# Kernel tuning notes

Hardware: AMD Instinct MI355X
Metric: run time of the kernel (lower is better)

The kernel has to match this reference:

```python
import jax, jax.numpy as jnp
import numpy as np

N_NODES = 20000
N_GRAPH = 256
NODE_DIM = 128
MULS = (128, 64, 32)       # node irreps: 128x0e + 64x1o + 32x2e
HC = 32                    # hidden channels per irrep
HIDDEN_DIM = 64
N_PATH = 9                 # feasible uuw paths into 0e+1e+2e
W_NUMEL = N_PATH * HC * HC # 9216


def _tables():
    # real Clebsch-Gordan tensors built from cartesian tensor algebra,
    # normalized so that sum(C**2) = 2*l_out + 1 (component normalization)
    eps = np.zeros((3, 3, 3))
    eps[0, 1, 2] = eps[1, 2, 0] = eps[2, 0, 1] = 1.0
    eps[0, 2, 1] = eps[2, 1, 0] = eps[1, 0, 2] = -1.0
    s2, s6 = 1 / np.sqrt(2), 1 / np.sqrt(6)
    Q2 = np.zeros((5, 3, 3))  # orthonormal basis of traceless symmetric 3x3
    Q2[0, 0, 1] = Q2[0, 1, 0] = s2          # xy
    Q2[1, 1, 2] = Q2[1, 2, 1] = s2          # yz
    Q2[2, 0, 0] = Q2[2, 1, 1] = -s6; Q2[2, 2, 2] = 2 * s6  # z2
    Q2[3, 0, 2] = Q2[3, 2, 0] = s2          # xz
    Q2[4, 0, 0] = s2; Q2[4, 1, 1] = -s2     # x2-y2

    def nrm(C, l3):
        return C * np.sqrt((2 * l3 + 1) / (C ** 2).sum())

    C000 = np.ones((1, 1, 1))
    C022 = np.eye(5)[None, :, :]
    C110 = np.eye(3).reshape(3, 3, 1) / np.sqrt(3)
    C111 = eps / np.sqrt(2)
    C112 = np.transpose(Q2, (1, 2, 0))
    C202 = np.eye(5)[:, None, :]
    C220 = np.eye(5).reshape(5, 5, 1) / np.sqrt(5)
    M = np.einsum('iab,jdb->ijad', Q2, Q2)  # [5,5,3,3]
    C221 = nrm(np.einsum('cad,ijad->ijc', eps, M), 1)
    S = 0.5 * (M + np.transpose(M, (0, 1, 3, 2)))
    S = S - np.trace(S, axis1=2, axis2=3)[..., None, None] * np.eye(3) / 3.0
    C222 = nrm(np.einsum('kad,ijad->ijk', Q2, S), 2)
    # sph2cart change of basis: 9 spherical comps (0e+1e+2e) -> 3x3 cartesian
    Qc = np.zeros((3, 3, 9))
    Qc[:, :, 0] = np.eye(3) / np.sqrt(3)        # isotropic part
    Qc[:, :, 1:4] = eps / np.sqrt(2)            # antisymmetric part
    Qc[:, :, 4:9] = np.transpose(Q2, (1, 2, 0)) # symmetric traceless part
    return [C000, C022, C110, C111, C112, C202, C220, C221, C222], Qc

_CGS, _QC = _tables()


def setup_inputs() -> dict:
    key = jax.random.key(0)
    ks = jax.random.split(key, 12)
    f32 = jnp.float32
    d_sph = MULS[0] + 3 * MULS[1] + 5 * MULS[2]  # 480
    return {
        'x_scalar': jax.random.normal(ks[0], (N_NODES, NODE_DIM), f32),
        'x_spherical': jax.random.normal(ks[1], (N_NODES, d_sph), f32),
        'batch': jnp.sort(jax.random.randint(ks[2], (N_NODES,), 0, N_GRAPH)),
        'W0e': jax.random.normal(ks[3], (MULS[0], HC), f32),
        'W1o': jax.random.normal(ks[4], (MULS[1], HC), f32),
        'W2e': jax.random.normal(ks[5], (MULS[2], HC), f32),
        'Wm1': jax.random.normal(ks[6], (NODE_DIM, HIDDEN_DIM), f32) / np.sqrt(NODE_DIM),
        'bm1': jnp.zeros((HIDDEN_DIM,), f32),
        'Wm2': jax.random.normal(ks[7], (HIDDEN_DIM, W_NUMEL), f32) / np.sqrt(HIDDEN_DIM),
        'bm2': jnp.zeros((W_NUMEL,), f32),
        'P0': jax.random.normal(ks[8], (3 * HC,), f32),
        'P1': jax.random.normal(ks[9], (2 * HC,), f32),
        'P2': jax.random.normal(ks[10], (4 * HC,), f32),
    }


def reference(x_scalar, x_spherical, batch, W0e, W1o, W2e, Wm1, bm1, Wm2, bm2, P0, P1, P2):
    n = x_scalar.shape[0]
    m0, m1, m2 = MULS
    # split node features into irrep blocks
    x0 = x_spherical[:, :m0, None]                        # [N,128,1] 0e
    x1 = x_spherical[:, m0:m0 + 3 * m1].reshape(n, m1, 3) # [N,64,3]  1o
    x2 = x_spherical[:, m0 + 3 * m1:].reshape(n, m2, 5)   # [N,32,5]  2e
    # pre_lin: per-irrep channel mixing (e3nn-style 1/sqrt(fan_in))
    h = [jnp.einsum('num,uv->nvm', x, W) / np.sqrt(W.shape[0])
         for x, W in ((x0, W0e), (x1, W1o), (x2, W2e))]   # each [N,32,2l+1]
    # per-node tensor-product weights from scalar features
    w = (jax.nn.silu(x_scalar @ Wm1 + bm1) @ Wm2 + bm2).reshape(n, N_PATH, HC, HC)
    # uuw tensor product, path order matches _CGS
    paths = ((0, 0), (0, 2), (1, 1), (1, 1), (1, 1), (2, 0), (2, 2), (2, 2), (2, 2))
    inv_u = 1.0 / np.sqrt(HC)
    outs = []
    for k, (i, j) in enumerate(paths):
        C = jnp.asarray(_CGS[k], x_scalar.dtype)
        outs.append(jnp.einsum('pqr,nup,nuq,nuw->nwr', C, h[i], h[j], w[:, k]) * inv_u)
    # post_lin: combine paths of each output l into a single channel
    y0 = jnp.einsum('num,u->nm', jnp.concatenate([outs[0], outs[2], outs[6]], 1), P0) / np.sqrt(3 * HC)
    y1 = jnp.einsum('num,u->nm', jnp.concatenate([outs[3], outs[7]], 1), P1) / np.sqrt(2 * HC)
    y2 = jnp.einsum('num,u->nm', jnp.concatenate([outs[1], outs[4], outs[5], outs[8]], 1), P2) / np.sqrt(4 * HC)
    sph = jnp.concatenate([y0, y1, y2], axis=1)           # [N,9]
    cart = jnp.einsum('abi,ni->nab', jnp.asarray(_QC, sph.dtype), sph)  # [N,3,3]
    red = jax.ops.segment_sum(cart, batch, num_segments=N_GRAPH)        # [B,3,3]
    # if_trace is False (if_iso=False): roll every non-batch dim by 1
    return jnp.roll(jnp.roll(red, 1, axis=1), 1, axis=2)
```

## Files before the change

### kernel.cpp

```cpp
#include <hip/hip_runtime.h>
#include <math.h>

#define OFF_W2P 0
#define OFF_B2P 14336
#define WS_FLOATS 14592

#define SC_Y0 0.0180421959121758f
#define SC_Y2 0.015625f
#define S2f 0.70710678118654752f
#define S6f 0.40824829046386302f
#define TWOS2f 1.41421356237309505f
#define TWOS6f 0.81649658092772603f
#define ISQRT3 0.57735026918962576f
#define ISQRT5 0.44721359549995794f
#define H0SC 0.08838834764831845f
#define H1SC 0.125f
#define H2SC 0.17677669529663689f

__device__ __constant__ int KARR[7] = {0, 1, 2, 4, 5, 6, 8};

__global__ __launch_bounds__(256) void prep_kernel(
    const float* __restrict__ Wm2, const float* __restrict__ bm2,
    const float* __restrict__ P0, const float* __restrict__ P2,
    float* __restrict__ ws, float* __restrict__ out) {
  int j = blockIdx.x * 256 + threadIdx.x;
  if (j < 2304) out[j] = 0.f;

  if (j < 14336) {
    int s = j >> 11; int rem = j & 2047; int c = rem >> 5; int u = rem & 31;
    int k = KARR[s];
    const float* P;
    float sc;
    switch (s) {
      case 0: P = P0;      sc = SC_Y0; break;
      case 1: P = P2;      sc = SC_Y2; break;
      case 2: P = P0 + 32; sc = SC_Y0; break;
      case 3: P = P2 + 32; sc = SC_Y2; break;
      case 4: P = P2 + 64; sc = SC_Y2; break;
      case 5: P = P0 + 64; sc = SC_Y0; break;
      default: P = P2 + 96; sc = SC_Y2; break;
    }
    const float4* w4 = (const float4*)(Wm2 + c * 9216 + k * 1024 + u * 32);
    const float4* p4 = (const float4*)P;
    float acc = 0.f;
#pragma unroll
    for (int q = 0; q < 8; ++q) {
      float4 a = w4[q], b = p4[q];
      acc += a.x * b.x + a.y * b.y + a.z * b.z + a.w * b.w;
    }
    ws[OFF_W2P + c * 224 + s * 32 + u] = acc * sc;
  } else if (j < 14560) {
    int i = j - 14336; int s = i >> 5; int u = i & 31; int k = KARR[s];
    const float* P;
    float sc;
    switch (s) {
      case 0: P = P0;      sc = SC_Y0; break;
      case 1: P = P2;      sc = SC_Y2; break;
      case 2: P = P0 + 32; sc = SC_Y0; break;
      case 3: P = P2 + 32; sc = SC_Y2; break;
      case 4: P = P2 + 64; sc = SC_Y2; break;
      case 5: P = P0 + 64; sc = SC_Y0; break;
      default: P = P2 + 96; sc = SC_Y2; break;
    }
    const float* b = bm2 + k * 1024 + u * 32;
    float acc = 0.f;
#pragma unroll
    for (int w = 0; w < 32; ++w) acc += b[w] * P[w];
    ws[OFF_B2P + s * 32 + u] = acc * sc;
  }
}

__global__ __launch_bounds__(256, 3) void fused_kernel(
    const float* __restrict__ xs_g, const float* __restrict__ xsph,
    const float* __restrict__ W0e, const float* __restrict__ W1o,
    const float* __restrict__ W2e,
    const float* __restrict__ Wm1, const float* __restrict__ bm1,
    const float* __restrict__ ws, const int* __restrict__ batch,
    float* __restrict__ out, const float norm2) {
  __shared__ __align__(16) char smem[50560];
  float (*xs)[132] = (float (*)[132])smem;
  float (*Vt)[228] = (float (*)[228])smem;
  float (*xp)[484] = (float (*)[484])(smem + 14592);
  float (*hiT)[18] = (float (*)[18])(smem + 45568);
  float (*sphs)[6] = (float (*)[6])(smem + 50176);

  const int tid = threadIdx.x;
  const int n0 = blockIdx.x * 16;

  for (int idx = tid; idx < 512; idx += 256) {
    const int row = idx >> 5, c4 = idx & 31;
    *(float4*)&xs[row][c4 * 4] = *(const float4*)(xs_g + (size_t)(n0 + row) * 128 + c4 * 4);
  }
  for (int idx = tid; idx < 1920; idx += 256) {
    const int row = idx / 120, c4 = idx % 120;
    *(float4*)&xp[row][c4 * 4] = *(const float4*)(xsph + (size_t)(n0 + row) * 480 + c4 * 4);
  }
  __syncthreads();

  {
    const int n = tid >> 4, c0 = (tid & 15) * 4;
    float acc[4] = {0.f, 0.f, 0.f, 0.f};
#pragma unroll 4
    for (int mq = 0; mq < 32; ++mq) {
      const float4 xv = *(float4*)&xs[n][mq * 4];
      const float xa[4] = {xv.x, xv.y, xv.z, xv.w};
#pragma unroll
      for (int r = 0; r < 4; ++r) {
        const float4 w = *(const float4*)(Wm1 + (mq * 4 + r) * 64 + c0);
        const float xr = xa[r];
        acc[0] += xr * w.x; acc[1] += xr * w.y;
        acc[2] += xr * w.z; acc[3] += xr * w.w;
      }
    }
    const float4 bb = *(const float4*)(bm1 + c0);
    const float ba[4] = {bb.x, bb.y, bb.z, bb.w};
#pragma unroll
    for (int jj = 0; jj < 4; ++jj) {
      const float z = acc[jj] + ba[jj];
      hiT[c0 + jj][n] = z / (1.f + __expf(-z));
    }
  }
  __syncthreads();

  if (tid < 224) {
    const int og = tid >> 3, ng = tid & 7;
    const int o0 = og * 8, nl = ng * 2;
    const float4 blo = *(const float4*)(ws + OFF_B2P + o0);
    const float4 bhi = *(const float4*)(ws + OFF_B2P + o0 + 4);
    float acc[2][8];
#pragma unroll
    for (int i = 0; i < 2; ++i) {
      acc[i][0] = blo.x; acc[i][1] = blo.y; acc[i][2] = blo.z; acc[i][3] = blo.w;
      acc[i][4] = bhi.x; acc[i][5] = bhi.y; acc[i][6] = bhi.z; acc[i][7] = bhi.w;
    }
#pragma unroll 2
    for (int c = 0; c < 64; ++c) {
      const float2 hv = *(float2*)&hiT[c][nl];
      const float4 wlo = *(const float4*)(ws + OFF_W2P + c * 224 + o0);
      const float4 whi = *(const float4*)(ws + OFF_W2P + c * 224 + o0 + 4);
      const float hvv[2] = {hv.x, hv.y};
      const float wv[8] = {wlo.x, wlo.y, wlo.z, wlo.w, whi.x, whi.y, whi.z, whi.w};
#pragma unroll
      for (int i = 0; i < 2; ++i)
#pragma unroll
        for (int jj = 0; jj < 8; ++jj) acc[i][jj] += hvv[i] * wv[jj];
    }
#pragma unroll
    for (int i = 0; i < 2; ++i) {
      float4 a = {acc[i][0], acc[i][1], acc[i][2], acc[i][3]};
      float4 b = {acc[i][4], acc[i][5], acc[i][6], acc[i][7]};
      *(float4*)&Vt[nl + i][o0] = a;
      *(float4*)&Vt[nl + i][o0 + 4] = b;
    }
  }
  __syncthreads();

  const int u = tid & 31, ni = tid >> 5;

  float h0v[2] = {0.f, 0.f};
#pragma unroll 4
  for (int mq = 0; mq < 32; ++mq) {
    const float4 va = *(float4*)&xp[ni][mq * 4];
    const float4 vb = *(float4*)&xp[ni + 8][mq * 4];
    const float xa[4] = {va.x, va.y, va.z, va.w};
    const float xb[4] = {vb.x, vb.y, vb.z, vb.w};
#pragma unroll
    for (int r = 0; r < 4; ++r) {
      const float w = W0e[(mq * 4 + r) * 32 + u];
      h0v[0] += xa[r] * w;
      h0v[1] += xb[r] * w;
    }
  }
  h0v[0] *= H0SC; h0v[1] *= H0SC;

  float h1v[2][3] = {{0.f, 0.f, 0.f}, {0.f, 0.f, 0.f}};
#pragma unroll 2
  for (int mq = 0; mq < 16; ++mq) {
    const float4 a0 = *(float4*)&xp[ni][128 + mq * 12];
    const float4 a1 = *(float4*)&xp[ni][128 + mq * 12 + 4];
    const float4 a2 = *(float4*)&xp[ni][128 + mq * 12 + 8];
    const float4 b0 = *(float4*)&xp[ni + 8][128 + mq * 12];
    const float4 b1 = *(float4*)&xp[ni + 8][128 + mq * 12 + 4];
    const float4 b2 = *(float4*)&xp[ni + 8][128 + mq * 12 + 8];
    const float xa[12] = {a0.x, a0.y, a0.z, a0.w, a1.x, a1.y, a1.z, a1.w,
                          a2.x, a2.y, a2.z, a2.w};
    const float xb[12] = {b0.x, b0.y, b0.z, b0.w, b1.x, b1.y, b1.z, b1.w,
                          b2.x, b2.y, b2.z, b2.w};
#pragma unroll
    for (int mm = 0; mm < 4; ++mm) {
      const float w = W1o[(mq * 4 + mm) * 32 + u];
#pragma unroll
      for (int j = 0; j < 3; ++j) {
        h1v[0][j] += xa[mm * 3 + j] * w;
        h1v[1][j] += xb[mm * 3 + j] * w;
      }
    }
  }
#pragma unroll
  for (int j = 0; j < 3; ++j) { h1v[0][j] *= H1SC; h1v[1][j] *= H1SC; }

  float h2r[2][5] = {{0.f, 0.f, 0.f, 0.f, 0.f}, {0.f, 0.f, 0.f, 0.f, 0.f}};
#pragma unroll 2
  for (int mq = 0; mq < 8; ++mq) {
    const float4 a0 = *(float4*)&xp[ni][320 + mq * 20];
    const float4 a1 = *(float4*)&xp[ni][320 + mq * 20 + 4];
    const float4 a2 = *(float4*)&xp[ni][320 + mq * 20 + 8];
    const float4 a3 = *(float4*)&xp[ni][320 + mq * 20 + 12];
    const float4 a4 = *(float4*)&xp[ni][320 + mq * 20 + 16];
    const float4 b0 = *(float4*)&xp[ni + 8][320 + mq * 20];
    const float4 b1 = *(float4*)&xp[ni + 8][320 + mq * 20 + 4];
    const float4 b2 = *(float4*)&xp[ni + 8][320 + mq * 20 + 8];
    const float4 b3 = *(float4*)&xp[ni + 8][320 + mq * 20 + 12];
    const float4 b4 = *(float4*)&xp[ni + 8][320 + mq * 20 + 16];
    const float xa[20] = {a0.x, a0.y, a0.z, a0.w, a1.x, a1.y, a1.z, a1.w,
                          a2.x, a2.y, a2.z, a2.w, a3.x, a3.y, a3.z, a3.w,
                          a4.x, a4.y, a4.z, a4.w};
    const float xb[20] = {b0.x, b0.y, b0.z, b0.w, b1.x, b1.y, b1.z, b1.w,
                          b2.x, b2.y, b2.z, b2.w, b3.x, b3.y, b3.z, b3.w,
                          b4.x, b4.y, b4.z, b4.w};
#pragma unroll
    for (int mm = 0; mm < 4; ++mm) {
      const float w = W2e[(mq * 4 + mm) * 32 + u];
#pragma unroll
      for (int j = 0; j < 5; ++j) {
        h2r[0][j] += xa[mm * 5 + j] * w;
        h2r[1][j] += xb[mm * 5 + j] * w;
      }
    }
  }
#pragma unroll
  for (int j = 0; j < 5; ++j) { h2r[0][j] *= H2SC; h2r[1][j] *= H2SC; }

#pragma unroll
  for (int it = 0; it < 2; ++it) {
    const int ln = ni + 8 * it;
    const float* Vp = &Vt[ln][u];
    const float v0 = Vp[0], v1 = Vp[32], v2 = Vp[64], v3 = Vp[96];
    const float v4 = Vp[128], v5 = Vp[160], v6 = Vp[192];
    const float h0 = h0v[it];
    const float h1a = h1v[it][0], h1b = h1v[it][1], h1c = h1v[it][2];
    float h2v[5];
#pragma unroll
    for (int j = 0; j < 5; ++j) h2v[j] = h2r[it][j];

    const float d11 = h1a * h1a + h1b * h1b + h1c * h1c;
    const float d22 = h2v[0] * h2v[0] + h2v[1] * h2v[1] + h2v[2] * h2v[2] +
                      h2v[3] * h2v[3] + h2v[4] * h2v[4];
    float y0 = v0 * h0 * h0 + v2 * d11 * ISQRT3 + v5 * d22 * ISQRT5;

    const float o00 = h1a * h1a, o01 = h1a * h1b, o02 = h1a * h1c;
    const float o11 = h1b * h1b, o12 = h1b * h1c, o22 = h1c * h1c;
    const float t40 = TWOS2f * o01, t41 = TWOS2f * o12;
    const float t42 = S6f * (2.f * o22 - o00 - o11);
    const float t43 = TWOS2f * o02, t44 = S2f * (o00 - o11);

    const float A00 = -S6f * h2v[2] + S2f * h2v[4];
    const float A01 = S2f * h2v[0];
    const float A02 = S2f * h2v[3];
    const float A11 = -S6f * h2v[2] - S2f * h2v[4];
    const float A12 = S2f * h2v[1];
    const float A22 = TWOS6f * h2v[2];
    const float B00 = A00 * A00 + A01 * A01 + A02 * A02;
    const float B01 = A00 * A01 + A01 * A11 + A02 * A12;
    const float B02 = A00 * A02 + A01 * A12 + A02 * A22;
    const float B11 = A01 * A01 + A11 * A11 + A12 * A12;
    const float B12 = A01 * A02 + A11 * A12 + A12 * A22;
    const float B22 = A02 * A02 + A12 * A12 + A22 * A22;
    const float t80 = TWOS2f * B01, t81 = TWOS2f * B12;
    const float t82 = S6f * (2.f * B22 - B00 - B11);
    const float t83 = TWOS2f * B02, t84 = S2f * (B00 - B11);

    const float w15 = (v1 + v4) * h0;
    const float v6n = v6 * norm2;
    float y2r[5];
    y2r[0] = w15 * h2v[0] + v3 * t40 + v6n * t80;
    y2r[1] = w15 * h2v[1] + v3 * t41 + v6n * t81;
    y2r[2] = w15 * h2v[2] + v3 * t42 + v6n * t82;
    y2r[3] = w15 * h2v[3] + v3 * t43 + v6n * t83;
    y2r[4] = w15 * h2v[4] + v3 * t44 + v6n * t84;

#pragma unroll
    for (int off = 16; off > 0; off >>= 1) {
      y0 += __shfl_xor(y0, off, 32);
#pragma unroll
      for (int r = 0; r < 5; ++r) y2r[r] += __shfl_xor(y2r[r], off, 32);
    }

    if (u == 0) {
      sphs[ln][0] = y0;
#pragma unroll
      for (int r = 0; r < 5; ++r) sphs[ln][1 + r] = y2r[r];
    }
  }
  __syncthreads();

  if (tid < 9) {
    const float QW[9][6] = {
        {ISQRT3, 0.f, 0.f, -S6f, 0.f, S2f},
        {0.f, S2f, 0.f, 0.f, 0.f, 0.f},
        {0.f, 0.f, 0.f, 0.f, S2f, 0.f},
        {0.f, S2f, 0.f, 0.f, 0.f, 0.f},
        {ISQRT3, 0.f, 0.f, -S6f, 0.f, -S2f},
        {0.f, 0.f, S2f, 0.f, 0.f, 0.f},
        {0.f, 0.f, 0.f, 0.f, S2f, 0.f},
        {0.f, 0.f, S2f, 0.f, 0.f, 0.f},
        {ISQRT3, 0.f, 0.f, TWOS6f, 0.f, 0.f}};
    const int a = tid / 3, b = tid % 3;
    const int rolled = ((a + 1) % 3) * 3 + ((b + 1) % 3);
    const float c0 = QW[tid][0], c1 = QW[tid][1], c2 = QW[tid][2];
    const float c3 = QW[tid][3], c4 = QW[tid][4], c5 = QW[tid][5];
    int cur_g = batch[n0];
    float acc = 0.f;
#pragma unroll
    for (int q = 0; q < 16; ++q) {
      const int g = batch[n0 + q];
      const float val = c0 * sphs[q][0] + c1 * sphs[q][1] + c2 * sphs[q][2] +
                        c3 * sphs[q][3] + c4 * sphs[q][4] + c5 * sphs[q][5];
      if (g != cur_g) {
        atomicAdd(out + cur_g * 9 + rolled, acc);
        acc = 0.f;
        cur_g = g;
      }
      acc += val;
    }
    atomicAdd(out + cur_g * 9 + rolled, acc);
  }
}

extern "C" void kernel_launch(void* const* d_in, const int* in_sizes, int n_in,
                              void* d_out, int out_size, void* d_ws, size_t ws_size,
                              hipStream_t stream) {
  const float* x_scalar = (const float*)d_in[0];
  const float* x_sph    = (const float*)d_in[1];
  const int*   batch    = (const int*)d_in[2];
  const float* W0e      = (const float*)d_in[3];
  const float* W1o      = (const float*)d_in[4];
  const float* W2e      = (const float*)d_in[5];
  const float* Wm1      = (const float*)d_in[6];
  const float* bm1      = (const float*)d_in[7];
  const float* Wm2      = (const float*)d_in[8];
  const float* bm2      = (const float*)d_in[9];
  const float* P0       = (const float*)d_in[10];
  const float* P2       = (const float*)d_in[12];
  float* ws  = (float*)d_ws;
  float* out = (float*)d_out;

  if (ws_size < (size_t)WS_FLOATS * sizeof(float)) return;

  double Q2[5][3][3] = {};
  const double s2d = 0.70710678118654752440, s6d = 0.40824829046386301637;
  Q2[0][0][1] = Q2[0][1][0] = s2d;
  Q2[1][1][2] = Q2[1][2][1] = s2d;
  Q2[2][0][0] = Q2[2][1][1] = -s6d; Q2[2][2][2] = 2.0 * s6d;
  Q2[3][0][2] = Q2[3][2][0] = s2d;
  Q2[4][0][0] = s2d; Q2[4][1][1] = -s2d;
  double ss = 0.0;
  for (int i = 0; i < 5; ++i)
    for (int jj = 0; jj < 5; ++jj) {
      double S[3][3];
      for (int a = 0; a < 3; ++a)
        for (int d = 0; d < 3; ++d) {
          double m1 = 0, m2 = 0;
          for (int b = 0; b < 3; ++b) {
            m1 += Q2[i][a][b] * Q2[jj][d][b];
            m2 += Q2[i][d][b] * Q2[jj][a][b];
          }
          S[a][d] = 0.5 * (m1 + m2);
        }
      double tr = (S[0][0] + S[1][1] + S[2][2]) / 3.0;
      S[0][0] -= tr; S[1][1] -= tr; S[2][2] -= tr;
      for (int kk = 0; kk < 5; ++kk) {
        double cc = 0;
        for (int a = 0; a < 3; ++a)
          for (int d = 0; d < 3; ++d) cc += Q2[kk][a][d] * S[a][d];
        ss += cc * cc;
      }
    }
  const float norm2 = (float)sqrt(5.0 / ss);

  prep_kernel<<<57, 256, 0, stream>>>(Wm2, bm2, P0, P2, ws, out);
  fused_kernel<<<1250, 256, 0, stream>>>(x_scalar, x_sph, W0e, W1o, W2e,
                                         Wm1, bm1, ws, batch, out, norm2);
}
```

Baseline: 162.3 us.

## Drop shared-memory staging of inputs, read rows directly and keep V in registers

Removes the ~50KB shared-memory staging of x_scalar and x_spherical rows and reads them directly from global memory. The per-node weight projection V is now accumulated in registers, with each thread owning its channel u, instead of being written to a shared Vt tile; this also removes one barrier. Launch bounds are raised to 6 blocks per SM to exploit the much smaller LDS footprint. The cost is uncoalesced, redundant global loads of rows that were previously shared across threads, and more register pressure from the larger occupancy target.

After: 208.7 us. 28.5% more time.

```diff
diff --git a/kernel.cpp b/kernel.cpp
--- a/kernel.cpp
+++ b/kernel.cpp
@@ -70,46 +70,33 @@
   }
 }
 
-__global__ __launch_bounds__(256, 3) void fused_kernel(
+__global__ __launch_bounds__(256, 6) void fused_kernel(
     const float* __restrict__ xs_g, const float* __restrict__ xsph,
     const float* __restrict__ W0e, const float* __restrict__ W1o,
     const float* __restrict__ W2e,
     const float* __restrict__ Wm1, const float* __restrict__ bm1,
     const float* __restrict__ ws, const int* __restrict__ batch,
     float* __restrict__ out, const float norm2) {
-  __shared__ __align__(16) char smem[50560];
-  float (*xs)[132] = (float (*)[132])smem;
-  float (*Vt)[228] = (float (*)[228])smem;
-  float (*xp)[484] = (float (*)[484])(smem + 14592);
-  float (*hiT)[18] = (float (*)[18])(smem + 45568);
-  float (*sphs)[6] = (float (*)[6])(smem + 50176);
+  __shared__ float hiT[64][18];
+  __shared__ float sphs[16][6];
 
   const int tid = threadIdx.x;
   const int n0 = blockIdx.x * 16;
 
-  for (int idx = tid; idx < 512; idx += 256) {
-    const int row = idx >> 5, c4 = idx & 31;
-    *(float4*)&xs[row][c4 * 4] = *(const float4*)(xs_g + (size_t)(n0 + row) * 128 + c4 * 4);
-  }
-  for (int idx = tid; idx < 1920; idx += 256) {
-    const int row = idx / 120, c4 = idx % 120;
-    *(float4*)&xp[row][c4 * 4] = *(const float4*)(xsph + (size_t)(n0 + row) * 480 + c4 * 4);
-  }
-  __syncthreads();
-
   {
     const int n = tid >> 4, c0 = (tid & 15) * 4;
+    const float* xr = xs_g + (size_t)(n0 + n) * 128;
     float acc[4] = {0.f, 0.f, 0.f, 0.f};
 #pragma unroll 4
     for (int mq = 0; mq < 32; ++mq) {
-      const float4 xv = *(float4*)&xs[n][mq * 4];
+      const float4 xv = *(const float4*)(xr + mq * 4);
       const float xa[4] = {xv.x, xv.y, xv.z, xv.w};
 #pragma unroll
       for (int r = 0; r < 4; ++r) {
         const float4 w = *(const float4*)(Wm1 + (mq * 4 + r) * 64 + c0);
-        const float xr = xa[r];
-        acc[0] += xr * w.x; acc[1] += xr * w.y;
-        acc[2] += xr * w.z; acc[3] += xr * w.w;
+        const float xr_ = xa[r];
+        acc[0] += xr_ * w.x; acc[1] += xr_ * w.y;
+        acc[2] += xr_ * w.z; acc[3] += xr_ * w.w;
       }
     }
     const float4 bb = *(const float4*)(bm1 + c0);
@@ -122,121 +109,95 @@
   }
   __syncthreads();
 
-  if (tid < 224) {
-    const int og = tid >> 3, ng = tid & 7;
-    const int o0 = og * 8, nl = ng * 2;
-    const float4 blo = *(const float4*)(ws + OFF_B2P + o0);
-    const float4 bhi = *(const float4*)(ws + OFF_B2P + o0 + 4);
-    float acc[2][8];
-#pragma unroll
-    for (int i = 0; i < 2; ++i) {
-      acc[i][0] = blo.x; acc[i][1] = blo.y; acc[i][2] = blo.z; acc[i][3] = blo.w;
-      acc[i][4] = bhi.x; acc[i][5] = bhi.y; acc[i][6] = bhi.z; acc[i][7] = bhi.w;
-    }
+  const int u = tid & 31, ni = tid >> 5;
+
+  float h0v[2];
+  float h1v[2][3];
+  float h2r[2][5];
+#pragma unroll
+  for (int it = 0; it < 2; ++it) {
+    const float* row = xsph + (size_t)(n0 + ni + 8 * it) * 480;
+
+    {
+      float a0 = 0.f;
+#pragma unroll 4
+      for (int mq = 0; mq < 32; ++mq) {
+        const float4 xv = *(const float4*)(row + mq * 4);
+        const float xa[4] = {xv.x, xv.y, xv.z, xv.w};
+#pragma unroll
+        for (int r = 0; r < 4; ++r) a0 += xa[r] * W0e[(mq * 4 + r) * 32 + u];
+      }
+      h0v[it] = a0 * H0SC;
+    }
+
+    {
+      float a1[3] = {0.f, 0.f, 0.f};
 #pragma unroll 2
-    for (int c = 0; c < 64; ++c) {
-      const float2 hv = *(float2*)&hiT[c][nl];
-      const float4 wlo = *(const float4*)(ws + OFF_W2P + c * 224 + o0);
-      const float4 whi = *(const float4*)(ws + OFF_W2P + c * 224 + o0 + 4);
-      const float hvv[2] = {hv.x, hv.y};
-      const float wv[8] = {wlo.x, wlo.y, wlo.z, wlo.w, whi.x, whi.y, whi.z, whi.w};
-#pragma unroll
-      for (int i = 0; i < 2; ++i)
-#pragma unroll
-        for (int jj = 0; jj < 8; ++jj) acc[i][jj] += hvv[i] * wv[jj];
-    }
-#pragma unroll
-    for (int i = 0; i < 2; ++i) {
-      float4 a = {acc[i][0], acc[i][1], acc[i][2], acc[i][3]};
-      float4 b = {acc[i][4], acc[i][5], acc[i][6], acc[i][7]};
-      *(float4*)&Vt[nl + i][o0] = a;
-      *(float4*)&Vt[nl + i][o0 + 4] = b;
-    }
-  }
-  __syncthreads();
-
-  const int u = tid & 31, ni = tid >> 5;
-
-  float h0v[2] = {0.f, 0.f};
+      for (int mq = 0; mq < 16; ++mq) {
+        const float4 b0 = *(const float4*)(row + 128 + mq * 12);
+        const float4 b1 = *(const float4*)(row + 128 + mq * 12 + 4);
+        const float4 b2 = *(const float4*)(row + 128 + mq * 12 + 8);
+        const float xa[12] = {b0.x, b0.y, b0.z, b0.w, b1.x, b1.y, b1.z, b1.w,
+                              b2.x, b2.y, b2.z, b2.w};
+#pragma unroll
+        for (int mm = 0; mm < 4; ++mm) {
+          const float w = W1o[(mq * 4 + mm) * 32 + u];
+#pragma unroll
+          for (int j = 0; j < 3; ++j) a1[j] += xa[mm * 3 + j] * w;
+        }
+      }
+#pragma unroll
+      for (int j = 0; j < 3; ++j) h1v[it][j] = a1[j] * H1SC;
+    }
+
+    {
+      float a2[5] = {0.f, 0.f, 0.f, 0.f, 0.f};
+#pragma unroll 2
+      for (int mq = 0; mq < 8; ++mq) {
+        const float4 c0v = *(const float4*)(row + 320 + mq * 20);
+        const float4 c1v = *(const float4*)(row + 320 + mq * 20 + 4);
+        const float4 c2v = *(const float4*)(row + 320 + mq * 20 + 8);
+        const float4 c3v = *(const float4*)(row + 320 + mq * 20 + 12);
+        const float4 c4v = *(const float4*)(row + 320 + mq * 20 + 16);
+        const float xa[20] = {c0v.x, c0v.y, c0v.z, c0v.w, c1v.x, c1v.y, c1v.z, c1v.w,
+                              c2v.x, c2v.y, c2v.z, c2v.w, c3v.x, c3v.y, c3v.z, c3v.w,
+                              c4v.x, c4v.y, c4v.z, c4v.w};
+#pragma unroll
+        for (int mm = 0; mm < 4; ++mm) {
+          const float w = W2e[(mq * 4 + mm) * 32 + u];
+#pragma unroll
+          for (int j = 0; j < 5; ++j) a2[j] += xa[mm * 5 + j] * w;
+        }
+      }
+#pragma unroll
+      for (int j = 0; j < 5; ++j) h2r[it][j] = a2[j] * H2SC;
+    }
+  }
+
+  float vv[2][7];
+#pragma unroll
+  for (int s = 0; s < 7; ++s) {
+    const float b = ws[OFF_B2P + s * 32 + u];
+    vv[0][s] = b; vv[1][s] = b;
+  }
 #pragma unroll 4
-  for (int mq = 0; mq < 32; ++mq) {
-    const float4 va = *(float4*)&xp[ni][mq * 4];
-    const float4 vb = *(float4*)&xp[ni + 8][mq * 4];
-    const float xa[4] = {va.x, va.y, va.z, va.w};
-    const float xb[4] = {vb.x, vb.y, vb.z, vb.w};
-#pragma unroll
-    for (int r = 0; r < 4; ++r) {
-      const float w = W0e[(mq * 4 + r) * 32 + u];
-      h0v[0] += xa[r] * w;
-      h0v[1] += xb[r] * w;
-    }
-  }
-  h0v[0] *= H0SC; h0v[1] *= H0SC;
-
-  float h1v[2][3] = {{0.f, 0.f, 0.f}, {0.f, 0.f, 0.f}};
-#pragma unroll 2
-  for (int mq = 0; mq < 16; ++mq) {
-    const float4 a0 = *(float4*)&xp[ni][128 + mq * 12];
-    const float4 a1 = *(float4*)&xp[ni][128 + mq * 12 + 4];
-    const float4 a2 = *(float4*)&xp[ni][128 + mq * 12 + 8];
-    const float4 b0 = *(float4*)&xp[ni + 8][128 + mq * 12];
-    const float4 b1 = *(float4*)&xp[ni + 8][128 + mq * 12 + 4];
-    const float4 b2 = *(float4*)&xp[ni + 8][128 + mq * 12 + 8];
-    const float xa[12] = {a0.x, a0.y, a0.z, a0.w, a1.x, a1.y, a1.z, a1.w,
-                          a2.x, a2.y, a2.z, a2.w};
-    const float xb[12] = {b0.x, b0.y, b0.z, b0.w, b1.x, b1.y, b1.z, b1.w,
-                          b2.x, b2.y, b2.z, b2.w};
-#pragma unroll
-    for (int mm = 0; mm < 4; ++mm) {
-      const float w = W1o[(mq * 4 + mm) * 32 + u];
-#pragma unroll
-      for (int j = 0; j < 3; ++j) {
-        h1v[0][j] += xa[mm * 3 + j] * w;
-        h1v[1][j] += xb[mm * 3 + j] * w;
-      }
-    }
-  }
-#pragma unroll
-  for (int j = 0; j < 3; ++j) { h1v[0][j] *= H1SC; h1v[1][j] *= H1SC; }
-
-  float h2r[2][5] = {{0.f, 0.f, 0.f, 0.f, 0.f}, {0.f, 0.f, 0.f, 0.f, 0.f}};
-#pragma unroll 2
-  for (int mq = 0; mq < 8; ++mq) {
-    const float4 a0 = *(float4*)&xp[ni][320 + mq * 20];
-    const float4 a1 = *(float4*)&xp[ni][320 + mq * 20 + 4];
-    const float4 a2 = *(float4*)&xp[ni][320 + mq * 20 + 8];
-    const float4 a3 = *(float4*)&xp[ni][320 + mq * 20 + 12];
-    const float4 a4 = *(float4*)&xp[ni][320 + mq * 20 + 16];
-    const float4 b0 = *(float4*)&xp[ni + 8][320 + mq * 20];
-    const float4 b1 = *(float4*)&xp[ni + 8][320 + mq * 20 + 4];
-    const float4 b2 = *(float4*)&xp[ni + 8][320 + mq * 20 + 8];
-    const float4 b3 = *(float4*)&xp[ni + 8][320 + mq * 20 + 12];
-    const float4 b4 = *(float4*)&xp[ni + 8][320 + mq * 20 + 16];
-    const float xa[20] = {a0.x, a0.y, a0.z, a0.w, a1.x, a1.y, a1.z, a1.w,
-                          a2.x, a2.y, a2.z, a2.w, a3.x, a3.y, a3.z, a3.w,
-                          a4.x, a4.y, a4.z, a4.w};
-    const float xb[20] = {b0.x, b0.y, b0.z, b0.w, b1.x, b1.y, b1.z, b1.w,
-                          b2.x, b2.y, b2.z, b2.w, b3.x, b3.y, b3.z, b3.w,
-                          b4.x, b4.y, b4.z, b4.w};
-#pragma unroll
-    for (int mm = 0; mm < 4; ++mm) {
-      const float w = W2e[(mq * 4 + mm) * 32 + u];
-#pragma unroll
-      for (int j = 0; j < 5; ++j) {
-        h2r[0][j] += xa[mm * 5 + j] * w;
-        h2r[1][j] += xb[mm * 5 + j] * w;
-      }
-    }
-  }
-#pragma unroll
-  for (int j = 0; j < 5; ++j) { h2r[0][j] *= H2SC; h2r[1][j] *= H2SC; }
+  for (int c = 0; c < 64; ++c) {
+    const float ha = hiT[c][ni];
+    const float hb = hiT[c][ni + 8];
+    const float* wrow = ws + OFF_W2P + c * 224 + u;
+#pragma unroll
+    for (int s = 0; s < 7; ++s) {
+      const float w = wrow[s * 32];
+      vv[0][s] += ha * w;
+      vv[1][s] += hb * w;
+    }
+  }
 
 #pragma unroll
   for (int it = 0; it < 2; ++it) {
     const int ln = ni + 8 * it;
-    const float* Vp = &Vt[ln][u];
-    const float v0 = Vp[0], v1 = Vp[32], v2 = Vp[64], v3 = Vp[96];
-    const float v4 = Vp[128], v5 = Vp[160], v6 = Vp[192];
+    const float v0 = vv[it][0], v1 = vv[it][1], v2 = vv[it][2], v3 = vv[it][3];
+    const float v4 = vv[it][4], v5 = vv[it][5], v6 = vv[it][6];
     const float h0 = h0v[it];
     const float h1a = h1v[it][0], h1b = h1v[it][1], h1c = h1v[it][2];
     float h2v[5];
```
